# Performance work log

Measured on AMD Instinct MI355X. Metric: run time of the kernel, lower is better.

The kernel has to match this reference:

```python
import jax, jax.numpy as jnp
import numpy as np

D = 2048        # input_size / model dim
H = 2816        # hidden_size per expert (GLU -> w1 has 2*H rows)
E = 8           # num_experts
M = 4096        # tokens (batch*seq)


def setup_inputs() -> dict:
    key = jax.random.key(0)
    k1, k2, k3, k4, k5 = jax.random.split(key, 5)
    x = jax.random.normal(k1, (M, D), dtype=jnp.float32)
    # ParallelExperts init: uniform(-1/fan_in_dim, 1/fan_in_dim); scale kept simple here
    w1 = jax.random.uniform(k2, (E, 2 * H, D), dtype=jnp.float32, minval=-1.0, maxval=1.0) / (2 * H)
    w2 = jax.random.uniform(k3, (E, D, H), dtype=jnp.float32, minval=-1.0, maxval=1.0) / D
    router_w = jax.random.normal(k4, (E, D), dtype=jnp.float32) * (1.0 / np.sqrt(D))
    bias = jnp.zeros((D,), dtype=jnp.float32)
    return {"x": x, "w1": w1, "w2": w2, "router_w": router_w, "bias": bias, "top_k": 2}


def _moe_forward(x, w1, w2, router_w, bias, top_k):
    # Router: logits -> softmax (fp32) -> top-k -> renormalize (fused_moe semantics)
    logits = x @ router_w.T                                # [M, E]
    probs = jax.nn.softmax(logits.astype(jnp.float32), axis=-1)
    topk_w, topk_ids = jax.lax.top_k(probs, top_k)         # [M, k]
    topk_w = topk_w / jnp.sum(topk_w, axis=-1, keepdims=True)
    # Dense combine weights [M, E]: gate weight if expert selected, else 0
    m = x.shape[0]
    combine = jnp.zeros((m, w1.shape[0]), dtype=x.dtype)
    combine = combine.at[jnp.arange(m)[:, None], topk_ids].add(topk_w.astype(x.dtype))
    # Grouped expert GEMMs, expressed as a loop over the small fixed expert set.
    # Contribution of expert e is masked by combine[:, e] (zero for unrouted tokens).
    y = jnp.zeros_like(x)
    hdim = w2.shape[2]
    for e in range(w1.shape[0]):
        g = x @ w1[e].T                                    # [M, 2H]
        h = jax.nn.silu(g[:, :hdim]) * g[:, hdim:]          # silu_and_mul (GLU)
        y = y + combine[:, e:e + 1] * (h @ w2[e].T)         # [M, D]
    return y + bias


def reference(x, w1, w2, router_w, bias, top_k):
    return _moe_forward(x, w1, w2, router_w, bias, top_k)
```

## Files before the change

### kernel.cpp

```cpp
#include <hip/hip_runtime.h>
#include <hip/hip_bf16.h>
#include <stdint.h>

#define M_TOK 4096
#define DDIM  2048
#define HDIM  2816
#define NEXP  8
#define PMAX  10240
#define MAXTILES 40
#define NB1   22
#define NB2   8
#define NKT1  32
#define NKT2  44

typedef __attribute__((ext_vector_type(8))) short short8;
typedef __attribute__((ext_vector_type(4))) float f32x4;

#define GLD16(g, l) __builtin_amdgcn_global_load_lds(                              \
    (const __attribute__((address_space(1))) unsigned int*)(g),                    \
    (__attribute__((address_space(3))) unsigned int*)(l), 16, 0, 0)

#define VMCNT(n) asm volatile("s_waitcnt vmcnt(" #n ")" ::: "memory")

__device__ __forceinline__ unsigned short f2bf(float f) {
  unsigned int u = __float_as_uint(f);
  u += 0x7fffu + ((u >> 16) & 1u);
  return (unsigned short)(u >> 16);
}
__device__ __forceinline__ float bf2f(unsigned short u) {
  return __uint_as_float(((unsigned)u) << 16);
}


#define STGA(TT, PP, S)                                                            \
  { size_t kb_ = (size_t)(TT) * 128 + (S) * 64;                                    \
    char* d_ = ldsp + (PP) * 32768 + (S) * 16384;                                  \
    GLD16(aS0 + kb_, d_ + tid * 16); GLD16(aS1 + kb_, d_ + 8192 + tid * 16); }

#define STGB(TT, PP, S)                                                            \
  { size_t kb_ = (size_t)(TT) * 128 + (S) * 64;                                    \
    char* d_ = ldsp + 65536 + (PP) * 32768 + (S) * 16384;                          \
    GLD16(bS0 + kb_, d_ + tid * 16); GLD16(bS1 + kb_, d_ + 8192 + tid * 16); }

#define DSRA(PP, S, M)                                                             \
  { const char* ab_ = ldsp + (PP) * 32768 + (S) * 16384;                           \
    _Pragma("unroll") for (int j_ = 0; j_ < 4; ++j_)                               \
      av[j_] = *(const short8*)(ab_ + aoff[(M) * 4 + j_]); }

#define DSRB(PP, S)                                                                \
  { const char* bb_ = ldsp + 65536 + (PP) * 32768 + (S) * 16384;                   \
    _Pragma("unroll") for (int j_ = 0; j_ < 4; ++j_)                               \
      bv[j_] = *(const short8*)(bb_ + boff[j_]); }

#define MMA16(M)                                                                   \
  { __builtin_amdgcn_s_setprio(1);                                                 \
    _Pragma("unroll") for (int j_ = 0; j_ < 4; ++j_)                               \
      _Pragma("unroll") for (int n_ = 0; n_ < 4; ++n_)                             \
        acc[(M) * 4 + j_][n_] =                                                    \
          __builtin_amdgcn_mfma_f32_16x16x32_bf16(av[j_], bv[n_], acc[(M)*4+j_][n_], 0, 0, 0); \
    __builtin_amdgcn_s_setprio(0); }

#define KTILE(T, P, S0, S1, S2, S3, VM)                                            \
  {                       \
    DSRA(P, 0, 0); DSRB(P, 0);                                                     \
    if (S0) STGA((T) + 1, (P) ^ 1, 1);                                             \
    __builtin_amdgcn_s_barrier(); MMA16(0); __builtin_amdgcn_s_barrier();          \
                          \
    DSRA(P, 0, 1);                                                                 \
    if (S1) STGB((T) + 2, P, 0);                                                   \
    __builtin_amdgcn_s_barrier(); MMA16(1); __builtin_amdgcn_s_barrier();          \
                          \
    DSRA(P, 1, 0); DSRB(P, 1);                                                     \
    if (S2) STGA((T) + 2, P, 0);                                                   \
    __builtin_amdgcn_s_barrier(); MMA16(0); __builtin_amdgcn_s_barrier();          \
        \
    DSRA(P, 1, 1);                                                                 \
    if (S3) STGB((T) + 2, P, 1);                                                   \
    __builtin_amdgcn_s_barrier(); MMA16(1);                                        \
    VMCNT(VM);                                                                     \
    __builtin_amdgcn_s_barrier(); }

__global__ void cvt_bf16_k(const float4* __restrict__ in, ushort4* __restrict__ out, int n4) {
  int stride = gridDim.x * blockDim.x;
  for (int i = blockIdx.x * blockDim.x + threadIdx.x; i < n4; i += stride) {
    float4 v = in[i];
    ushort4 o;
    o.x = f2bf(v.x); o.y = f2bf(v.y); o.z = f2bf(v.z); o.w = f2bf(v.w);
    out[i] = o;
  }
}

__global__ void init_k(int* __restrict__ tok, int* __restrict__ counts, int* __restrict__ cursors) {
  int i = blockIdx.x * blockDim.x + threadIdx.x;
  if (i < PMAX) tok[i] = -1;
  if (i < NEXP) { counts[i] = 0; cursors[i] = 0; }
}

__global__ __launch_bounds__(256) void router_k(const float4* __restrict__ x4,
                                                const float4* __restrict__ rw4,
                                                ushort4* __restrict__ xb4,
                                                float* __restrict__ wgt,
                                                int* __restrict__ eid,
                                                int* __restrict__ counts) {
  int lane = threadIdx.x & 63;
  int wv = threadIdx.x >> 6;
  int t = blockIdx.x * 4 + wv;
  int base = t * (DDIM / 4);
  float acc[NEXP];
#pragma unroll
  for (int e = 0; e < NEXP; ++e) acc[e] = 0.f;
#pragma unroll
  for (int j = 0; j < DDIM / 4 / 64; ++j) {
    float4 v = x4[base + j * 64 + lane];
    ushort4 o;
    o.x = f2bf(v.x); o.y = f2bf(v.y); o.z = f2bf(v.z); o.w = f2bf(v.w);
    xb4[base + j * 64 + lane] = o;
#pragma unroll
    for (int e = 0; e < NEXP; ++e) {
      float4 w = rw4[e * (DDIM / 4) + j * 64 + lane];
      acc[e] += v.x * w.x + v.y * w.y + v.z * w.z + v.w * w.w;
    }
  }
#pragma unroll
  for (int e = 0; e < NEXP; ++e) {
#pragma unroll
    for (int s = 32; s > 0; s >>= 1) acc[e] += __shfl_xor(acc[e], s, 64);
  }
  if (lane == 0) {
    float mx = acc[0];
#pragma unroll
    for (int e = 1; e < NEXP; ++e) mx = fmaxf(mx, acc[e]);
    float p[NEXP];
#pragma unroll
    for (int e = 0; e < NEXP; ++e) p[e] = expf(acc[e] - mx);
    int e0 = 0; float p0 = p[0];
#pragma unroll
    for (int e = 1; e < NEXP; ++e) if (p[e] > p0) { p0 = p[e]; e0 = e; }
    int e1 = -1; float p1 = -1.f;
#pragma unroll
    for (int e = 0; e < NEXP; ++e) if (e != e0 && p[e] > p1) { p1 = p[e]; e1 = e; }
    float s = p0 + p1;
    wgt[2 * t] = p0 / s; wgt[2 * t + 1] = p1 / s;
    eid[2 * t] = e0;     eid[2 * t + 1] = e1;
    atomicAdd(&counts[e0], 1);
    atomicAdd(&counts[e1], 1);
  }
}

__global__ void offsets_k(const int* __restrict__ counts, int* __restrict__ offs,
                          int* __restrict__ tile2exp, int* __restrict__ tilerow,
                          int* __restrict__ ntiles) {
  if (threadIdx.x == 0 && blockIdx.x == 0) {
    int o = 0, nt = 0;
    for (int e = 0; e < NEXP; ++e) {
      offs[e] = o;
      int c = counts[e];
      int pt = (c + 255) >> 8;
      for (int i = 0; i < pt; ++i) { tile2exp[nt] = e; tilerow[nt] = o + i * 256; ++nt; }
      o += pt << 8;
    }
    offs[NEXP] = o;
    ntiles[0] = nt;
  }
}

__global__ void scatter_k(const int* __restrict__ eid, const int* __restrict__ offs,
                          int* __restrict__ cursors, int* __restrict__ tok,
                          int* __restrict__ slot) {
  int t = blockIdx.x * blockDim.x + threadIdx.x;
  if (t >= M_TOK) return;
#pragma unroll
  for (int k = 0; k < 2; ++k) {
    int e = eid[2 * t + k];
    int p = offs[e] + atomicAdd(&cursors[e], 1);
    tok[p] = t;
    slot[2 * t + k] = p;
  }
}

__global__ __launch_bounds__(512, 1) void gemm1_k(const unsigned short* __restrict__ xb,
                                                  const unsigned short* __restrict__ w1b,
                                                  const int* __restrict__ tok,
                                                  const int* __restrict__ tile2exp,
                                                  const int* __restrict__ tilerow,
                                                  const int* __restrict__ ntiles,
                                                  unsigned short* __restrict__ h) {
  __shared__ char ldsp[131072];
  int mt = blockIdx.x;
  if (mt >= ntiles[0]) return;
  int e = tile2exp[mt], r0 = tilerow[mt];
  int n0 = blockIdx.y * 128;
  int tid = threadIdx.x, lane = tid & 63;
  int wv = tid >> 6, wm = wv >> 2, wn = wv & 3;
  int l15 = lane & 15, g = lane >> 4;

  int row0 = tid >> 2, g0 = (tid & 3) ^ ((row0 >> 1) & 3);
  int row1 = row0 + 128;
  int t0 = tok[r0 + row0]; if (t0 < 0) t0 = 0;
  int t1 = tok[r0 + row1]; if (t1 < 0) t1 = 0;
  const char* aS0 = (const char*)xb + (size_t)t0 * (DDIM * 2) + g0 * 16;
  const char* aS1 = (const char*)xb + (size_t)t1 * (DDIM * 2) + g0 * 16;
  size_t w1r0 = (size_t)e * (2 * HDIM) + (size_t)(n0 + row0);
  size_t w1r1 = (size_t)e * (2 * HDIM) + (size_t)(HDIM + n0 + row0);
  const char* bS0 = (const char*)w1b + w1r0 * (DDIM * 2) + g0 * 16;
  const char* bS1 = (const char*)w1b + w1r1 * (DDIM * 2) + g0 * 16;

  int aoff[8], boff[4];
#pragma unroll
  for (int mi = 0; mi < 8; ++mi) {
    int r = wm * 128 + mi * 16 + l15;
    aoff[mi] = r * 64 + ((g ^ ((r >> 1) & 3)) << 4);
  }
#pragma unroll
  for (int ni = 0; ni < 4; ++ni) {
    int r = wn * 64 + ni * 16 + l15;
    boff[ni] = r * 64 + ((g ^ ((r >> 1) & 3)) << 4);
  }

  f32x4 acc[8][4];
#pragma unroll
  for (int mi = 0; mi < 8; ++mi)
#pragma unroll
    for (int ni = 0; ni < 4; ++ni) acc[mi][ni] = (f32x4)(0.f);

  short8 av[4], bv[4];

  STGA(0, 0, 0); STGB(0, 0, 0); STGA(0, 0, 1); STGB(0, 0, 1);
  STGB(1, 1, 0); STGA(1, 1, 0); STGB(1, 1, 1);
  VMCNT(6);
  __builtin_amdgcn_s_barrier();

#pragma unroll 1
  for (int t = 0; t < NKT1 - 2; t += 2) {
    KTILE(t, 0, 1, 1, 1, 1, 6);
    KTILE(t + 1, 1, 1, 1, 1, 1, 6);
  }
  KTILE(NKT1 - 2, 0, 1, 0, 0, 0, 0);
  KTILE(NKT1 - 1, 1, 0, 0, 0, 0, 0);

  __syncthreads();
  float* xch = (float*)ldsp;
  int rbase = (lane >> 4) * 4;
  if (wn >= 2) {
    int uc0 = (wn - 2) * 64;
#pragma unroll
    for (int mi = 0; mi < 8; ++mi)
#pragma unroll
      for (int ni = 0; ni < 4; ++ni)
#pragma unroll
        for (int j = 0; j < 4; ++j) {
          int r = wm * 128 + mi * 16 + rbase + j;
          int c = uc0 + ni * 16 + l15;
          int cs = c ^ ((r & 3) << 2) ^ ((r & 1) << 4);
          xch[r * 128 + cs] = acc[mi][ni][j];
        }
  }
  __syncthreads();
  if (wn < 2) {
#pragma unroll
    for (int mi = 0; mi < 8; ++mi)
#pragma unroll
      for (int ni = 0; ni < 4; ++ni)
#pragma unroll
        for (int j = 0; j < 4; ++j) {
          int r = wm * 128 + mi * 16 + rbase + j;
          int c = wn * 64 + ni * 16 + l15;
          int cs = c ^ ((r & 3) << 2) ^ ((r & 1) << 4);
          float gg = acc[mi][ni][j];
          float u = xch[r * 128 + cs];
          float sv = gg / (1.f + expf(-gg));
          h[(size_t)(r0 + r) * HDIM + n0 + c] = f2bf(sv * u);
        }
  }
}

__global__ __launch_bounds__(512, 1) void gemm2_k(const unsigned short* __restrict__ h,
                                                  const unsigned short* __restrict__ w2b,
                                                  const int* __restrict__ tile2exp,
                                                  const int* __restrict__ tilerow,
                                                  const int* __restrict__ ntiles,
                                                  unsigned short* __restrict__ yp) {
  __shared__ char ldsp[131072];
  int mt = blockIdx.x;
  if (mt >= ntiles[0]) return;
  int e = tile2exp[mt], r0 = tilerow[mt];
  int n0 = blockIdx.y * 256;
  int tid = threadIdx.x, lane = tid & 63;
  int wv = tid >> 6, wm = wv >> 2, wn = wv & 3;
  int l15 = lane & 15, g = lane >> 4;

  int row0 = tid >> 2, g0 = (tid & 3) ^ ((row0 >> 1) & 3);
  int row1 = row0 + 128;
  const char* aS0 = (const char*)h + (size_t)(r0 + row0) * (HDIM * 2) + g0 * 16;
  const char* aS1 = (const char*)h + (size_t)(r0 + row1) * (HDIM * 2) + g0 * 16;
  const char* bS0 = (const char*)w2b + ((size_t)e * DDIM + n0 + row0) * (HDIM * 2) + g0 * 16;
  const char* bS1 = (const char*)w2b + ((size_t)e * DDIM + n0 + row1) * (HDIM * 2) + g0 * 16;

  int aoff[8], boff[4];
#pragma unroll
  for (int mi = 0; mi < 8; ++mi) {
    int r = wm * 128 + mi * 16 + l15;
    aoff[mi] = r * 64 + ((g ^ ((r >> 1) & 3)) << 4);
  }
#pragma unroll
  for (int ni = 0; ni < 4; ++ni) {
    int r = wn * 64 + ni * 16 + l15;
    boff[ni] = r * 64 + ((g ^ ((r >> 1) & 3)) << 4);
  }

  f32x4 acc[8][4];
#pragma unroll
  for (int mi = 0; mi < 8; ++mi)
#pragma unroll
    for (int ni = 0; ni < 4; ++ni) acc[mi][ni] = (f32x4)(0.f);

  short8 av[4], bv[4];

  STGA(0, 0, 0); STGB(0, 0, 0); STGA(0, 0, 1); STGB(0, 0, 1);
  STGB(1, 1, 0); STGA(1, 1, 0); STGB(1, 1, 1);
  VMCNT(6);
  __builtin_amdgcn_s_barrier();

#pragma unroll 1
  for (int t = 0; t < NKT2 - 2; t += 2) {
    KTILE(t, 0, 1, 1, 1, 1, 6);
    KTILE(t + 1, 1, 1, 1, 1, 1, 6);
  }
  KTILE(NKT2 - 2, 0, 1, 0, 0, 0, 0);
  KTILE(NKT2 - 1, 1, 0, 0, 0, 0, 0);

  int rbase = (lane >> 4) * 4;
#pragma unroll
  for (int mi = 0; mi < 8; ++mi)
#pragma unroll
    for (int ni = 0; ni < 4; ++ni)
#pragma unroll
      for (int j = 0; j < 4; ++j) {
        int r = r0 + wm * 128 + mi * 16 + rbase + j;
        int c = n0 + wn * 64 + ni * 16 + l15;
        yp[(size_t)r * DDIM + c] = f2bf(acc[mi][ni][j]);
      }
}

__global__ void combine_k(const unsigned short* __restrict__ yp, const float* __restrict__ wgt,
                          const int* __restrict__ slot, const float* __restrict__ bias,
                          float* __restrict__ out) {
  int idx = blockIdx.x * blockDim.x + threadIdx.x;
  int t = idx >> 8, q = (idx & 255) * 8;
  float w0 = wgt[2 * t], w1 = wgt[2 * t + 1];
  int s0 = slot[2 * t], s1 = slot[2 * t + 1];
  short8 a8 = *(const short8*)(yp + (size_t)s0 * DDIM + q);
  short8 b8 = *(const short8*)(yp + (size_t)s1 * DDIM + q);
  float* op = out + (size_t)t * DDIM + q;
#pragma unroll
  for (int k = 0; k < 8; ++k) {
    float av = bf2f((unsigned short)a8[k]);
    float bv = bf2f((unsigned short)b8[k]);
    op[k] = w0 * av + w1 * bv + bias[q + k];
  }
}

extern "C" void kernel_launch(void* const* d_in, const int* in_sizes, int n_in,
                              void* d_out, int out_size, void* d_ws, size_t ws_size,
                              hipStream_t stream) {
  const float* x    = (const float*)d_in[0];
  const float* w1   = (const float*)d_in[1];
  const float* w2   = (const float*)d_in[2];
  const float* rw   = (const float*)d_in[3];
  const float* bias = (const float*)d_in[4];
  float* out = (float*)d_out;

  char* ws = (char*)d_ws;
  size_t off = 0;
  auto alloc = [&](size_t bytes) -> void* {
    void* p = ws + off;
    off = (off + bytes + 255) & ~(size_t)255;
    return p;
  };
  unsigned short* w1b = (unsigned short*)alloc((size_t)NEXP * 2 * HDIM * DDIM * 2);
  unsigned short* w2b = (unsigned short*)alloc((size_t)NEXP * DDIM * HDIM * 2);
  unsigned short* xb  = (unsigned short*)alloc((size_t)M_TOK * DDIM * 2);
  unsigned short* h   = (unsigned short*)alloc((size_t)PMAX * HDIM * 2);
  unsigned short* yp  = (unsigned short*)alloc((size_t)PMAX * DDIM * 2);
  float* wgt          = (float*)alloc((size_t)M_TOK * 2 * 4);
  int* eid            = (int*)alloc((size_t)M_TOK * 2 * 4);
  int* slot           = (int*)alloc((size_t)M_TOK * 2 * 4);
  int* tok            = (int*)alloc((size_t)PMAX * 4);
  int* counts         = (int*)alloc(64 * 4);
  int* cursors        = (int*)alloc(64 * 4);
  int* offs           = (int*)alloc(64 * 4);
  int* ntiles         = (int*)alloc(64 * 4);
  int* tile2exp       = (int*)alloc(128 * 4);
  int* tilerow        = (int*)alloc(128 * 4);

  hipLaunchKernelGGL(init_k, dim3((PMAX + 255) / 256), dim3(256), 0, stream, tok, counts, cursors);
  hipLaunchKernelGGL(cvt_bf16_k, dim3(2048), dim3(256), 0, stream,
                     (const float4*)w1, (ushort4*)w1b, (int)((size_t)NEXP * 2 * HDIM * DDIM / 4));
  hipLaunchKernelGGL(cvt_bf16_k, dim3(2048), dim3(256), 0, stream,
                     (const float4*)w2, (ushort4*)w2b, (int)((size_t)NEXP * DDIM * HDIM / 4));
  hipLaunchKernelGGL(router_k, dim3(M_TOK / 4), dim3(256), 0, stream,
                     (const float4*)x, (const float4*)rw, (ushort4*)xb, wgt, eid, counts);
  hipLaunchKernelGGL(offsets_k, dim3(1), dim3(64), 0, stream, counts, offs,
                     tile2exp, tilerow, ntiles);
  hipLaunchKernelGGL(scatter_k, dim3((M_TOK + 255) / 256), dim3(256), 0, stream, eid, offs, cursors, tok, slot);
  hipLaunchKernelGGL(gemm1_k, dim3(MAXTILES, NB1), dim3(512), 0, stream,
                     xb, w1b, tok, tile2exp, tilerow, ntiles, h);
  hipLaunchKernelGGL(gemm2_k, dim3(MAXTILES, NB2), dim3(512), 0, stream,
                     h, w2b, tile2exp, tilerow, ntiles, yp);
  hipLaunchKernelGGL(combine_k, dim3(M_TOK * (DDIM / 8) / 256), dim3(256), 0, stream, yp, wgt, slot, bias, out);
}
```

Before: 750.6 us.

## Fold weight conversion into router kernel and retile gemm2 to 256x128 blocks

The fp32-to-bf16 conversions of w1 and w2 move into the router kernel as a grid-stride tail, removing two launches. gemm2 is rewritten from a 512-thread 256x256 tile with a double-buffered multi-stage LDS pipeline to a 256-thread 256x128 tile with 48KB single-buffered LDS, a new XOR swizzle, and two blocks per CU. The aim is higher occupancy and more blocks for the second GEMM. The cost is that the per-k-step load is no longer overlapped with MFMA work (a full vmcnt(0) wait each iteration), and the weight conversion now runs after the router work in each block.

Result: no change. 757.5 us (+0.9%).

```diff
diff --git a/kernel.cpp b/kernel.cpp
--- a/kernel.cpp
+++ b/kernel.cpp
@@ -9,7 +9,7 @@
 #define PMAX  10240
 #define MAXTILES 40
 #define NB1   22
-#define NB2   8
+#define NB2   16
 #define NKT1  32
 #define NKT2  44
 
@@ -30,7 +30,6 @@
 __device__ __forceinline__ float bf2f(unsigned short u) {
   return __uint_as_float(((unsigned)u) << 16);
 }
-
 
 #define STGA(TT, PP, S)                                                            \
   { size_t kb_ = (size_t)(TT) * 128 + (S) * 64;                                    \
@@ -61,47 +60,37 @@
     __builtin_amdgcn_s_setprio(0); }
 
 #define KTILE(T, P, S0, S1, S2, S3, VM)                                            \
-  {                       \
-    DSRA(P, 0, 0); DSRB(P, 0);                                                     \
+  { DSRA(P, 0, 0); DSRB(P, 0);                                                     \
     if (S0) STGA((T) + 1, (P) ^ 1, 1);                                             \
     __builtin_amdgcn_s_barrier(); MMA16(0); __builtin_amdgcn_s_barrier();          \
-                          \
     DSRA(P, 0, 1);                                                                 \
     if (S1) STGB((T) + 2, P, 0);                                                   \
     __builtin_amdgcn_s_barrier(); MMA16(1); __builtin_amdgcn_s_barrier();          \
-                          \
     DSRA(P, 1, 0); DSRB(P, 1);                                                     \
     if (S2) STGA((T) + 2, P, 0);                                                   \
     __builtin_amdgcn_s_barrier(); MMA16(0); __builtin_amdgcn_s_barrier();          \
-        \
     DSRA(P, 1, 1);                                                                 \
     if (S3) STGB((T) + 2, P, 1);                                                   \
     __builtin_amdgcn_s_barrier(); MMA16(1);                                        \
     VMCNT(VM);                                                                     \
     __builtin_amdgcn_s_barrier(); }
 
-__global__ void cvt_bf16_k(const float4* __restrict__ in, ushort4* __restrict__ out, int n4) {
-  int stride = gridDim.x * blockDim.x;
-  for (int i = blockIdx.x * blockDim.x + threadIdx.x; i < n4; i += stride) {
-    float4 v = in[i];
-    ushort4 o;
-    o.x = f2bf(v.x); o.y = f2bf(v.y); o.z = f2bf(v.z); o.w = f2bf(v.w);
-    out[i] = o;
-  }
-}
-
 __global__ void init_k(int* __restrict__ tok, int* __restrict__ counts, int* __restrict__ cursors) {
   int i = blockIdx.x * blockDim.x + threadIdx.x;
   if (i < PMAX) tok[i] = -1;
   if (i < NEXP) { counts[i] = 0; cursors[i] = 0; }
 }
 
-__global__ __launch_bounds__(256) void router_k(const float4* __restrict__ x4,
-                                                const float4* __restrict__ rw4,
-                                                ushort4* __restrict__ xb4,
-                                                float* __restrict__ wgt,
-                                                int* __restrict__ eid,
-                                                int* __restrict__ counts) {
+__global__ __launch_bounds__(256) void router_cvt_k(const float4* __restrict__ x4,
+                                                    const float4* __restrict__ rw4,
+                                                    ushort4* __restrict__ xb4,
+                                                    float* __restrict__ wgt,
+                                                    int* __restrict__ eid,
+                                                    int* __restrict__ counts,
+                                                    const float4* __restrict__ w14,
+                                                    ushort4* __restrict__ w1b4,
+                                                    const float4* __restrict__ w24,
+                                                    ushort4* __restrict__ w2b4) {
   int lane = threadIdx.x & 63;
   int wv = threadIdx.x >> 6;
   int t = blockIdx.x * 4 + wv;
@@ -144,6 +133,22 @@
     eid[2 * t] = e0;     eid[2 * t + 1] = e1;
     atomicAdd(&counts[e0], 1);
     atomicAdd(&counts[e1], 1);
+  }
+  const int n1 = NEXP * 2 * HDIM * DDIM / 4;
+  const int n2 = NEXP * DDIM * HDIM / 4;
+  const int stride = (M_TOK / 4) * 256;
+  int id = blockIdx.x * 256 + threadIdx.x;
+  for (int i = id; i < n1; i += stride) {
+    float4 v = w14[i];
+    ushort4 o;
+    o.x = f2bf(v.x); o.y = f2bf(v.y); o.z = f2bf(v.z); o.w = f2bf(v.w);
+    w1b4[i] = o;
+  }
+  for (int i = id; i < n2; i += stride) {
+    float4 v = w24[i];
+    ushort4 o;
+    o.x = f2bf(v.x); o.y = f2bf(v.y); o.z = f2bf(v.z); o.w = f2bf(v.w);
+    w2b4[i] = o;
   }
 }
 
@@ -274,38 +279,44 @@
   }
 }
 
-__global__ __launch_bounds__(512, 1) void gemm2_k(const unsigned short* __restrict__ h,
+__global__ __launch_bounds__(256, 2) void gemm2_k(const unsigned short* __restrict__ h,
                                                   const unsigned short* __restrict__ w2b,
                                                   const int* __restrict__ tile2exp,
                                                   const int* __restrict__ tilerow,
                                                   const int* __restrict__ ntiles,
                                                   unsigned short* __restrict__ yp) {
-  __shared__ char ldsp[131072];
+  __shared__ char ldsp[49152];
   int mt = blockIdx.x;
   if (mt >= ntiles[0]) return;
   int e = tile2exp[mt], r0 = tilerow[mt];
-  int n0 = blockIdx.y * 256;
+  int n0 = blockIdx.y * 128;
   int tid = threadIdx.x, lane = tid & 63;
-  int wv = tid >> 6, wm = wv >> 2, wn = wv & 3;
-  int l15 = lane & 15, g = lane >> 4;
-
-  int row0 = tid >> 2, g0 = (tid & 3) ^ ((row0 >> 1) & 3);
-  int row1 = row0 + 128;
-  const char* aS0 = (const char*)h + (size_t)(r0 + row0) * (HDIM * 2) + g0 * 16;
-  const char* aS1 = (const char*)h + (size_t)(r0 + row1) * (HDIM * 2) + g0 * 16;
-  const char* bS0 = (const char*)w2b + ((size_t)e * DDIM + n0 + row0) * (HDIM * 2) + g0 * 16;
-  const char* bS1 = (const char*)w2b + ((size_t)e * DDIM + n0 + row1) * (HDIM * 2) + g0 * 16;
-
-  int aoff[8], boff[4];
-#pragma unroll
-  for (int mi = 0; mi < 8; ++mi) {
-    int r = wm * 128 + mi * 16 + l15;
-    aoff[mi] = r * 64 + ((g ^ ((r >> 1) & 3)) << 4);
-  }
-#pragma unroll
-  for (int ni = 0; ni < 4; ++ni) {
-    int r = wn * 64 + ni * 16 + l15;
-    boff[ni] = r * 64 + ((g ^ ((r >> 1) & 3)) << 4);
+  int wv = tid >> 6, wm = wv >> 1, wn = wv & 1;
+  int l15 = lane & 15, lq = lane >> 4;
+
+  int sg = tid & 7, srow = tid >> 3;
+  unsigned int aOff[8], bOff[4];
+#pragma unroll
+  for (int j = 0; j < 8; ++j) {
+    int r = j * 32 + srow;
+    aOff[j] = (unsigned int)(r0 + r) * (HDIM * 2) + (unsigned int)((sg ^ (r & 7)) << 4);
+  }
+#pragma unroll
+  for (int j = 0; j < 4; ++j) {
+    int r = j * 32 + srow;
+    bOff[j] = (unsigned int)(e * DDIM + n0 + r) * (HDIM * 2) + (unsigned int)((sg ^ (r & 7)) << 4);
+  }
+
+  int aRd[8], bRd[4];
+#pragma unroll
+  for (int i = 0; i < 8; ++i) {
+    int r = wm * 128 + i * 16 + l15;
+    aRd[i] = r * 128 + ((lq ^ (r & 7)) << 4);
+  }
+#pragma unroll
+  for (int i = 0; i < 4; ++i) {
+    int r = wn * 64 + i * 16 + l15;
+    bRd[i] = r * 128 + ((lq ^ (r & 7)) << 4);
   }
 
   f32x4 acc[8][4];
@@ -314,29 +325,44 @@
 #pragma unroll
     for (int ni = 0; ni < 4; ++ni) acc[mi][ni] = (f32x4)(0.f);
 
-  short8 av[4], bv[4];
-
-  STGA(0, 0, 0); STGB(0, 0, 0); STGA(0, 0, 1); STGB(0, 0, 1);
-  STGB(1, 1, 0); STGA(1, 1, 0); STGB(1, 1, 1);
-  VMCNT(6);
-  __builtin_amdgcn_s_barrier();
+  const char* hB = (const char*)h;
+  const char* wB = (const char*)w2b;
 
 #pragma unroll 1
-  for (int t = 0; t < NKT2 - 2; t += 2) {
-    KTILE(t, 0, 1, 1, 1, 1, 6);
-    KTILE(t + 1, 1, 1, 1, 1, 1, 6);
-  }
-  KTILE(NKT2 - 2, 0, 1, 0, 0, 0, 0);
-  KTILE(NKT2 - 1, 1, 0, 0, 0, 0, 0);
-
-  int rbase = (lane >> 4) * 4;
+  for (int kt = 0; kt < NKT2; ++kt) {
+    __syncthreads();
+    unsigned int kb = (unsigned int)kt * 128;
+#pragma unroll
+    for (int j = 0; j < 8; ++j) GLD16(hB + aOff[j] + kb, ldsp + j * 4096 + tid * 16);
+#pragma unroll
+    for (int j = 0; j < 4; ++j) GLD16(wB + bOff[j] + kb, ldsp + 32768 + j * 4096 + tid * 16);
+    VMCNT(0);
+    __syncthreads();
+#pragma unroll
+    for (int kh = 0; kh < 2; ++kh) {
+      int kx = kh << 6;
+      short8 a[8], b[4];
+#pragma unroll
+      for (int i = 0; i < 8; ++i) a[i] = *(const short8*)(ldsp + (aRd[i] ^ kx));
+#pragma unroll
+      for (int i = 0; i < 4; ++i) b[i] = *(const short8*)(ldsp + 32768 + (bRd[i] ^ kx));
+      __builtin_amdgcn_s_setprio(1);
+#pragma unroll
+      for (int mi = 0; mi < 8; ++mi)
+#pragma unroll
+        for (int ni = 0; ni < 4; ++ni)
+          acc[mi][ni] = __builtin_amdgcn_mfma_f32_16x16x32_bf16(a[mi], b[ni], acc[mi][ni], 0, 0, 0);
+      __builtin_amdgcn_s_setprio(0);
+    }
+  }
+
 #pragma unroll
   for (int mi = 0; mi < 8; ++mi)
 #pragma unroll
     for (int ni = 0; ni < 4; ++ni)
 #pragma unroll
       for (int j = 0; j < 4; ++j) {
-        int r = r0 + wm * 128 + mi * 16 + rbase + j;
+        int r = r0 + wm * 128 + mi * 16 + lq * 4 + j;
         int c = n0 + wn * 64 + ni * 16 + l15;
         yp[(size_t)r * DDIM + c] = f2bf(acc[mi][ni][j]);
       }
@@ -394,18 +420,15 @@
   int* tilerow        = (int*)alloc(128 * 4);
 
   hipLaunchKernelGGL(init_k, dim3((PMAX + 255) / 256), dim3(256), 0, stream, tok, counts, cursors);
-  hipLaunchKernelGGL(cvt_bf16_k, dim3(2048), dim3(256), 0, stream,
-                     (const float4*)w1, (ushort4*)w1b, (int)((size_t)NEXP * 2 * HDIM * DDIM / 4));
-  hipLaunchKernelGGL(cvt_bf16_k, dim3(2048), dim3(256), 0, stream,
-                     (const float4*)w2, (ushort4*)w2b, (int)((size_t)NEXP * DDIM * HDIM / 4));
-  hipLaunchKernelGGL(router_k, dim3(M_TOK / 4), dim3(256), 0, stream,
-                     (const float4*)x, (const float4*)rw, (ushort4*)xb, wgt, eid, counts);
+  hipLaunchKernelGGL(router_cvt_k, dim3(M_TOK / 4), dim3(256), 0, stream,
+                     (const float4*)x, (const float4*)rw, (ushort4*)xb, wgt, eid, counts,
+                     (const float4*)w1, (ushort4*)w1b, (const float4*)w2, (ushort4*)w2b);
   hipLaunchKernelGGL(offsets_k, dim3(1), dim3(64), 0, stream, counts, offs,
                      tile2exp, tilerow, ntiles);
   hipLaunchKernelGGL(scatter_k, dim3((M_TOK + 255) / 256), dim3(256), 0, stream, eid, offs, cursors, tok, slot);
   hipLaunchKernelGGL(gemm1_k, dim3(MAXTILES, NB1), dim3(512), 0, stream,
                      xb, w1b, tok, tile2exp, tilerow, ntiles, h);
-  hipLaunchKernelGGL(gemm2_k, dim3(MAXTILES, NB2), dim3(512), 0, stream,
+  hipLaunchKernelGGL(gemm2_k, dim3(MAXTILES, NB2), dim3(256), 0, stream,
                      h, w2b, tile2exp, tilerow, ntiles, yp);
   hipLaunchKernelGGL(combine_k, dim3(M_TOK * (DDIM / 8) / 256), dim3(256), 0, stream, yp, wgt, slot, bias, out);
 }
```
